# Optimization experiments

Hardware: AMD Instinct MI355X
Metric: run time of the kernel (lower is better)

The kernel has to match this reference:

```python
import jax, jax.numpy as jnp
import numpy as np


def setup_inputs() -> dict:
    key = jax.random.key(0)
    k1, k2, k3 = jax.random.split(key, 3)
    B, T, I, H = 32, 2048, 512, 512
    x = jax.random.normal(k1, (B, T, I), dtype=jnp.float32)
    W_x = jax.random.normal(k2, (3, I, H), dtype=jnp.float32) / np.sqrt(I)
    W_h = jax.random.normal(k3, (3, H, H), dtype=jnp.float32) / np.sqrt(H)
    bias = jnp.zeros((3, H), dtype=jnp.float32)
    return {"x": x, "W_x": W_x, "W_h": W_h, "bias": bias}


def reference(x, W_x, W_h, bias):
    # x: [B, T, I]; W_x: [3, I, H]; W_h: [3, H, H]; bias: [3, H]
    B, T, I = x.shape
    H = W_h.shape[-1]
    # Precompute input-side contributions for all gates/timesteps (batched GEMM):
    # gx: [T, 3, B, H] = x @ W_x[g] + bias[g]
    gx = jnp.einsum('bti,gih->tgbh', x, W_x) + bias[:, None, :]

    W_hz, W_hr, W_hh = W_h[0], W_h[1], W_h[2]

    def step(h_prev, gx_t):
        # gx_t: [3, B, H]
        z = jax.nn.sigmoid(gx_t[0] + h_prev @ W_hz)          # update gate
        r = jax.nn.sigmoid(gx_t[1] + h_prev @ W_hr)          # reset gate
        h_tilde = jnp.tanh(gx_t[2] + (r * h_prev) @ W_hh)    # candidate
        h_t = (1.0 - z) * h_prev + z * h_tilde
        return h_t, h_t

    h0 = jnp.zeros((B, H), dtype=x.dtype)
    h_last, outs = jax.lax.scan(step, h0, gx)  # outs: [T, B, H]
    output = jnp.transpose(outs, (1, 0, 2))    # [B, T, H]
    return output, h_last
```

## Files before the change

kernel.cpp:

```cpp
#include <hip/hip_runtime.h>
#include <stdint.h>
#include <stddef.h>


#define AGENT __HIP_MEMORY_SCOPE_AGENT

typedef _Float16 h2v __attribute__((ext_vector_type(2)));
typedef _Float16 half8 __attribute__((ext_vector_type(8)));
typedef float f32x4 __attribute__((ext_vector_type(4)));

__device__ __forceinline__ uint32_t pk2u(float a, float b) {
  h2v r; r[0] = (_Float16)a; r[1] = (_Float16)b;
  return __builtin_bit_cast(uint32_t, r);
}
__device__ __forceinline__ h2v bc2(uint32_t u) { return __builtin_bit_cast(h2v, u); }
__device__ __forceinline__ float dot2f(h2v a, h2v b, float c) {
#if __has_builtin(__builtin_amdgcn_fdot2)
  return __builtin_amdgcn_fdot2(a, b, c, false);
#else
  return fmaf((float)a[1], (float)b[1], fmaf((float)a[0], (float)b[0], c));
#endif
}
__device__ __forceinline__ float sigmoidf_(float x) { return 1.0f / (1.0f + __expf(-x)); }
__device__ __forceinline__ float tanhf_(float x) { return 1.0f - 2.0f / (1.0f + __expf(2.0f * x)); }
__device__ __forceinline__ uint64_t ald64(const uint64_t* p) {
  return __hip_atomic_load(p, __ATOMIC_RELAXED, AGENT);
}
__device__ __forceinline__ void ast64(uint64_t* p, uint64_t v) {
  __hip_atomic_store(p, v, __ATOMIC_RELAXED, AGENT);
}

__global__ __launch_bounds__(256) void gemm_gx(const float* __restrict__ x,
                                               const float* __restrict__ Wx,
                                               const float* __restrict__ bias,
                                               _Float16* gzr,
                                               _Float16* gh,
                                               int nTN) {
  __shared__ alignas(16) _Float16 Alds[128 * 68];
  __shared__ alignas(16) _Float16 Blds[128 * 68];
  const int tid = threadIdx.x;
  const int bid = blockIdx.x;
  const int tm = bid / nTN, tn = bid % nTN;
  const int m0 = tm << 7, n0 = tn << 7;
  const int lane = tid & 63;
  const int wv = tid >> 6, wm = wv >> 1, wn = wv & 1;
  const int l15 = lane & 15, lhi = lane >> 4;
  f32x4 acc[4][4] = {};

  for (int k0 = 0; k0 < 512; k0 += 64) {
#pragma unroll
    for (int r = 0; r < 8; ++r) {
      int m = r * 16 + (tid >> 4);
      int k = (tid & 15) * 4;
      float4 v = *(const float4*)&x[(size_t)(m0 + m) * 512 + k0 + k];
      union { _Float16 h[4]; uint2 u; } cv;
      cv.h[0] = (_Float16)v.x; cv.h[1] = (_Float16)v.y;
      cv.h[2] = (_Float16)v.z; cv.h[3] = (_Float16)v.w;
      *(uint2*)&Alds[m * 68 + k] = cv.u;
    }
#pragma unroll
    for (int u = 0; u < 8; ++u) {
      int n = tid & 127;
      int k = (tid >> 7) * 32 + u * 4;
      int ng = n0 + n;
      const float* wp = Wx + ((size_t)(ng >> 9) << 18) + (size_t)(k0 + k) * 512 + (ng & 511);
      union { _Float16 h[4]; uint2 u2; } cv;
      cv.h[0] = (_Float16)wp[0];    cv.h[1] = (_Float16)wp[512];
      cv.h[2] = (_Float16)wp[1024]; cv.h[3] = (_Float16)wp[1536];
      *(uint2*)&Blds[n * 68 + k] = cv.u2;
    }
    __syncthreads();
#pragma unroll
    for (int kk = 0; kk < 2; ++kk) {
      int q = kk * 4 + lhi;
      half8 af[4], bf[4];
#pragma unroll
      for (int fm = 0; fm < 4; ++fm) {
        const _Float16* pa = &Alds[(wm * 64 + fm * 16 + l15) * 68 + q * 8];
        union { uint2 u[2]; half8 h; } cv;
        cv.u[0] = *(const uint2*)pa; cv.u[1] = *(const uint2*)(pa + 4);
        af[fm] = cv.h;
      }
#pragma unroll
      for (int fn = 0; fn < 4; ++fn) {
        const _Float16* pb = &Blds[(wn * 64 + fn * 16 + l15) * 68 + q * 8];
        union { uint2 u[2]; half8 h; } cv;
        cv.u[0] = *(const uint2*)pb; cv.u[1] = *(const uint2*)(pb + 4);
        bf[fn] = cv.h;
      }
#pragma unroll
      for (int fm = 0; fm < 4; ++fm)
#pragma unroll
        for (int fn = 0; fn < 4; ++fn)
          acc[fm][fn] = __builtin_amdgcn_mfma_f32_16x16x32_f16(af[fm], bf[fn], acc[fm][fn], 0, 0, 0);
    }
    __syncthreads();
  }
#pragma unroll
  for (int fn = 0; fn < 4; ++fn) {
    int col = n0 + wn * 64 + fn * 16 + l15;
    float bv = bias[col];
#pragma unroll
    for (int fm = 0; fm < 4; ++fm) {
#pragma unroll
      for (int q2 = 0; q2 < 4; ++q2) {
        int row = m0 + wm * 64 + fm * 16 + lhi * 4 + q2;
        _Float16 val = (_Float16)(acc[fm][fn][q2] + bv);
        if (n0 < 1024) gzr[(size_t)row * 1024 + col] = val;
        else           gh[(size_t)row * 512 + (col - 1024)] = val;
      }
    }
  }
}

template <bool GH>
__global__ __launch_bounds__(512) void gru_scan(
    const float* __restrict__ x,
    const float* __restrict__ Wx,
    const float* __restrict__ Wh,
    const float* __restrict__ bias,
    const _Float16* gzr,
    const _Float16* gh,
    float* out,
    uint64_t* __restrict__ Pbuf,
    uint64_t* __restrict__ zbuf) {
  __shared__ alignas(16) float zrp[2][8][64];
  __shared__ alignas(16) _Float16 wzr[2 * 64 * 516];
  __shared__ alignas(16) _Float16 h16[512];
  __shared__ alignas(16) _Float16 rh16[64];
  __shared__ alignas(16) _Float16 x16s[64];

  const int T = threadIdx.x;
  const int bid = blockIdx.x;
  const int xcd = bid & 7, ii = bid >> 3;
  const int batch = xcd * 4 + (ii >> 3);
  const int slice = ii & 7;
  const int wv = T >> 6;
  const int ln = T & 63;
  const int n = T;

  {
    const int cc = T & 63, kb = T >> 6;
#pragma unroll 4
    for (int g = 0; g < 2; ++g) {
      const float* W = Wh + (size_t)g * 262144 + slice * 64 + cc;
      for (int i = 0; i < 64; ++i) {
        int k = kb + 8 * i;
        wzr[(g * 64 + cc) * 516 + k] = (_Float16)W[(size_t)k * 512];
      }
    }
  }
  uint32_t wh2[32], wx2[GH ? 1 : 32];
  {
    const float* Whh = Wh + 524288;
#pragma unroll
    for (int j = 0; j < 32; ++j) {
      int kk = slice * 64 + 2 * j;
      wh2[j] = pk2u(Whh[(size_t)kk * 512 + n], Whh[(size_t)(kk + 1) * 512 + n]);
    }
    if (!GH) {
      const float* Wxh = Wx + 524288;
#pragma unroll
      for (int j = 0; j < 32; ++j) {
        int kk = slice * 64 + 2 * j;
        wx2[j] = pk2u(Wxh[(size_t)kk * 512 + n], Wxh[(size_t)(kk + 1) * 512 + n]);
      }
    }
  }
  const float bh = bias[1024 + n];

  float hreg = 0.0f;
  h16[T] = (_Float16)0.0f;

  const size_t rowbase = (size_t)batch * 2048;
  float gz_p = 0.f, gr_p = 0.f, gz_cur = 0.f, gr_cur = 0.f, x_p = 0.f;
  float gh_p = 0.f, gh_cur = 0.f;
  if (T < 64)       gz_p = (float)gzr[rowbase * 1024 + slice * 64 + T];
  else if (T < 128) gr_p = (float)gzr[rowbase * 1024 + 512 + slice * 64 + (T - 64)];
  if (GH) gh_p = (float)gh[rowbase * 512 + n];
  else if (T < 64) x_p = x[rowbase * 512 + slice * 64 + T];

  uint64_t* Pmine = Pbuf + ((size_t)batch * 8 + slice) * 512 + n;
  const uint64_t* Pread = Pbuf + ((size_t)batch * 8) * 512 + n;
  uint64_t* zmine = zbuf + (size_t)batch * 512 + slice * 64 + ln;
  const uint64_t* zread = zbuf + (size_t)batch * 512 + n;

  for (int t = 0; t < 2048; ++t) {
    if (t > 0) {
      const size_t po = ((t - 1) & 1) ? 131072 : 0;
      const size_t zo = ((t - 1) & 1) ? 16384 : 0;
      const uint32_t want = (uint32_t)t;
      uint64_t v[8];
#pragma unroll
      for (int g = 0; g < 8; ++g) v[g] = ald64(Pread + po + (size_t)g * 512);
      uint64_t zv = ald64(zread + zo);
      for (;;) {
        bool ok = true;
        if ((uint32_t)(zv >> 32) != want) { zv = ald64(zread + zo); ok = false; }
#pragma unroll
        for (int g = 0; g < 8; ++g)
          if ((uint32_t)(v[g] >> 32) != want) { v[g] = ald64(Pread + po + (size_t)g * 512); ok = false; }
        if (ok) break;
        __builtin_amdgcn_s_sleep(1);
      }
      float hsum = 0.f;
#pragma unroll
      for (int g = 0; g < 8; ++g) hsum += __uint_as_float((uint32_t)v[g]);
      float zf = __uint_as_float((uint32_t)zv);
      float htil = tanhf_(GH ? (gh_cur + hsum) : (bh + hsum));
      float hn = fmaf(zf, htil - hreg, hreg);
      if (slice == 0) out[(rowbase + (t - 1)) * 512 + n] = hn;
      hreg = hn;
      h16[T] = (_Float16)hn;
    }
    gz_cur = gz_p; gr_cur = gr_p;
    if (GH) gh_cur = gh_p;
    else if (T < 64) x16s[T] = (_Float16)x_p;
    __syncthreads();
    if (t < 2047) {
      size_t r1 = rowbase + t + 1;
      if (T < 64)       gz_p = (float)gzr[r1 * 1024 + slice * 64 + T];
      else if (T < 128) gr_p = (float)gzr[r1 * 1024 + 512 + slice * 64 + (T - 64)];
      if (GH) gh_p = (float)gh[r1 * 512 + n];
      else if (T < 64) x_p = x[r1 * 512 + slice * 64 + T];
    }

    float za = 0.f, ra = 0.f;
    {
      const _Float16* wzp = &wzr[(0 * 64 + ln) * 516 + 64 * wv];
      const _Float16* wrp = &wzr[(1 * 64 + ln) * 516 + 64 * wv];
      const _Float16* hp = &h16[64 * wv];
#pragma unroll
      for (int j = 0; j < 16; ++j) {
        uint2 wzu = *(const uint2*)(wzp + 4 * j);
        uint2 wru = *(const uint2*)(wrp + 4 * j);
        uint2 hu = *(const uint2*)(hp + 4 * j);
        za = dot2f(bc2(hu.x), bc2(wzu.x), za);
        za = dot2f(bc2(hu.y), bc2(wzu.y), za);
        ra = dot2f(bc2(hu.x), bc2(wru.x), ra);
        ra = dot2f(bc2(hu.y), bc2(wru.y), ra);
      }
    }
    zrp[0][wv][ln] = za;
    zrp[1][wv][ln] = ra;
    __syncthreads();
    const size_t po = (t & 1) ? 131072 : 0;
    const size_t zo = (t & 1) ? 16384 : 0;
    const uint64_t tagw = ((uint64_t)(uint32_t)(t + 1)) << 32;
    if (T < 128) {
      const int g = T >> 6, c = T & 63;
      float sum = 0.f;
#pragma unroll
      for (int s2 = 0; s2 < 8; ++s2) sum += zrp[g][s2][c];
      if (g == 0) {
        float z = sigmoidf_(sum + gz_cur);
        ast64(zmine + zo, tagw | (uint32_t)__float_as_uint(z));
      } else {
        float r = sigmoidf_(sum + gr_cur);
        rh16[c] = (_Float16)(r * (float)h16[slice * 64 + c]);
      }
    }
    __syncthreads();

    float pa = 0.f;
#pragma unroll
    for (int j = 0; j < 16; ++j) {
      uint2 ru = *(const uint2*)&rh16[4 * j];
      pa = dot2f(bc2(ru.x), bc2(wh2[2 * j]), pa);
      pa = dot2f(bc2(ru.y), bc2(wh2[2 * j + 1]), pa);
    }
    if (!GH) {
#pragma unroll
      for (int j = 0; j < 16; ++j) {
        uint2 xu = *(const uint2*)&x16s[4 * j];
        pa = dot2f(bc2(xu.x), bc2(wx2[2 * j]), pa);
        pa = dot2f(bc2(xu.y), bc2(wx2[2 * j + 1]), pa);
      }
    }
    ast64(Pmine + po, tagw | (uint32_t)__float_as_uint(pa));
    if (!GH) __syncthreads();
  }

  {
    const uint32_t want = 2048u;
    uint64_t v[8];
#pragma unroll
    for (int g = 0; g < 8; ++g) v[g] = ald64(Pread + 131072 + (size_t)g * 512);
    uint64_t zv = ald64(zread + 16384);
    for (;;) {
      bool ok = true;
      if ((uint32_t)(zv >> 32) != want) { zv = ald64(zread + 16384); ok = false; }
#pragma unroll
      for (int g = 0; g < 8; ++g)
        if ((uint32_t)(v[g] >> 32) != want) { v[g] = ald64(Pread + 131072 + (size_t)g * 512); ok = false; }
      if (ok) break;
      __builtin_amdgcn_s_sleep(1);
    }
    float hsum = 0.f;
#pragma unroll
    for (int g = 0; g < 8; ++g) hsum += __uint_as_float((uint32_t)v[g]);
    float zf = __uint_as_float((uint32_t)zv);
    float htil = tanhf_(GH ? (gh_cur + hsum) : (bh + hsum));
    float hn = fmaf(zf, htil - hreg, hreg);
    if (slice == 0) {
      out[(rowbase + 2047) * 512 + n] = hn;
      out[(size_t)32 * 2048 * 512 + (size_t)batch * 512 + n] = hn;
    }
  }
}

extern "C" void kernel_launch(void* const* d_in, const int* in_sizes, int n_in,
                              void* d_out, int out_size, void* d_ws, size_t ws_size,
                              hipStream_t stream) {
  (void)in_sizes; (void)n_in; (void)out_size;
  const float* x    = (const float*)d_in[0];
  const float* Wx   = (const float*)d_in[1];
  const float* Wh   = (const float*)d_in[2];
  const float* bias = (const float*)d_in[3];
  float* out = (float*)d_out;
  char* ws = (char*)d_ws;

  uint64_t* Pbuf = (uint64_t*)ws;
  uint64_t* zbuf = (uint64_t*)(ws + 2097152);
  _Float16* gh   = (_Float16*)(ws + 2621440);

  hipMemsetAsync(ws, 0, 2621440, stream);
  const bool gh_mode = ws_size >= (size_t)2621440 + 67108864ull;
  if (gh_mode) {
    gemm_gx<<<512 * 12, 256, 0, stream>>>(x, Wx, bias, (_Float16*)d_out, gh, 12);
    gru_scan<true><<<256, 512, 0, stream>>>(x, Wx, Wh, bias, (const _Float16*)d_out,
                                            gh, out, Pbuf, zbuf);
  } else {
    gemm_gx<<<512 * 8, 256, 0, stream>>>(x, Wx, bias, (_Float16*)d_out, gh, 8);
    gru_scan<false><<<256, 512, 0, stream>>>(x, Wx, Wh, bias, (const _Float16*)d_out,
                                             gh, out, Pbuf, zbuf);
  }
}
```

Before: 7.110 ms.

## Publish candidate partial before z-gate and poll with mostly workgroup-scope loads

Reorders the per-step work so the reset gate and candidate partial are computed and published first, and the update-gate matvec runs after publication. This takes z off the cross-block critical path. Polling now mostly uses workgroup-scope atomic loads, with an agent-scope load every eighth iteration, and publishes store at both workgroup and agent scope. The aim is to cut the cost of cross-CU spin-wait latency. The trade-offs are an extra store per publish and a reliance on scope semantics that may not make remote writes visible promptly, which could lengthen the waits.

```diff
diff --git a/kernel.cpp b/kernel.cpp
--- a/kernel.cpp
+++ b/kernel.cpp
@@ -4,6 +4,7 @@
 
 
 #define AGENT __HIP_MEMORY_SCOPE_AGENT
+#define WGSC  __HIP_MEMORY_SCOPE_WORKGROUP
 
 typedef _Float16 h2v __attribute__((ext_vector_type(2)));
 typedef _Float16 half8 __attribute__((ext_vector_type(8)));
@@ -23,10 +24,13 @@
 }
 __device__ __forceinline__ float sigmoidf_(float x) { return 1.0f / (1.0f + __expf(-x)); }
 __device__ __forceinline__ float tanhf_(float x) { return 1.0f - 2.0f / (1.0f + __expf(2.0f * x)); }
-__device__ __forceinline__ uint64_t ald64(const uint64_t* p) {
-  return __hip_atomic_load(p, __ATOMIC_RELAXED, AGENT);
-}
-__device__ __forceinline__ void ast64(uint64_t* p, uint64_t v) {
+
+__device__ __forceinline__ uint64_t ldT(const uint64_t* p, bool deep) {
+  return deep ? __hip_atomic_load(p, __ATOMIC_RELAXED, AGENT)
+              : __hip_atomic_load(p, __ATOMIC_RELAXED, WGSC);
+}
+__device__ __forceinline__ void pub2(uint64_t* p, uint64_t v) {
+  __hip_atomic_store(p, v, __ATOMIC_RELAXED, WGSC);
   __hip_atomic_store(p, v, __ATOMIC_RELAXED, AGENT);
 }
 
@@ -190,16 +194,16 @@
       const size_t po = ((t - 1) & 1) ? 131072 : 0;
       const size_t zo = ((t - 1) & 1) ? 16384 : 0;
       const uint32_t want = (uint32_t)t;
-      uint64_t v[8];
-#pragma unroll
-      for (int g = 0; g < 8; ++g) v[g] = ald64(Pread + po + (size_t)g * 512);
-      uint64_t zv = ald64(zread + zo);
+      uint64_t v[8] = {};
+      uint64_t zv = 0;
+      int it = 0;
       for (;;) {
         bool ok = true;
-        if ((uint32_t)(zv >> 32) != want) { zv = ald64(zread + zo); ok = false; }
+        bool deep = ((++it) & 7) == 0;
+        if ((uint32_t)(zv >> 32) != want) { zv = ldT(zread + zo, deep); ok = false; }
 #pragma unroll
         for (int g = 0; g < 8; ++g)
-          if ((uint32_t)(v[g] >> 32) != want) { v[g] = ald64(Pread + po + (size_t)g * 512); ok = false; }
+          if ((uint32_t)(v[g] >> 32) != want) { v[g] = ldT(Pread + po + (size_t)g * 512, deep); ok = false; }
         if (ok) break;
         __builtin_amdgcn_s_sleep(1);
       }
@@ -225,40 +229,31 @@
       else if (T < 64) x_p = x[r1 * 512 + slice * 64 + T];
     }
 
-    float za = 0.f, ra = 0.f;
-    {
-      const _Float16* wzp = &wzr[(0 * 64 + ln) * 516 + 64 * wv];
-      const _Float16* wrp = &wzr[(1 * 64 + ln) * 516 + 64 * wv];
-      const _Float16* hp = &h16[64 * wv];
-#pragma unroll
-      for (int j = 0; j < 16; ++j) {
-        uint2 wzu = *(const uint2*)(wzp + 4 * j);
-        uint2 wru = *(const uint2*)(wrp + 4 * j);
-        uint2 hu = *(const uint2*)(hp + 4 * j);
-        za = dot2f(bc2(hu.x), bc2(wzu.x), za);
-        za = dot2f(bc2(hu.y), bc2(wzu.y), za);
-        ra = dot2f(bc2(hu.x), bc2(wru.x), ra);
-        ra = dot2f(bc2(hu.y), bc2(wru.y), ra);
-      }
-    }
-    zrp[0][wv][ln] = za;
-    zrp[1][wv][ln] = ra;
-    __syncthreads();
     const size_t po = (t & 1) ? 131072 : 0;
     const size_t zo = (t & 1) ? 16384 : 0;
     const uint64_t tagw = ((uint64_t)(uint32_t)(t + 1)) << 32;
-    if (T < 128) {
-      const int g = T >> 6, c = T & 63;
+
+    float ra = 0.f;
+    {
+      const _Float16* wrp = &wzr[(64 + ln) * 516 + 64 * wv];
+      const _Float16* hp = &h16[64 * wv];
+#pragma unroll
+      for (int j = 0; j < 16; ++j) {
+        uint2 wru = *(const uint2*)(wrp + 4 * j);
+        uint2 hu = *(const uint2*)(hp + 4 * j);
+        ra = dot2f(bc2(hu.x), bc2(wru.x), ra);
+        ra = dot2f(bc2(hu.y), bc2(wru.y), ra);
+      }
+    }
+    zrp[1][wv][ln] = ra;
+    __syncthreads();
+    if (T >= 64 && T < 128) {
+      const int c = T - 64;
       float sum = 0.f;
 #pragma unroll
-      for (int s2 = 0; s2 < 8; ++s2) sum += zrp[g][s2][c];
-      if (g == 0) {
-        float z = sigmoidf_(sum + gz_cur);
-        ast64(zmine + zo, tagw | (uint32_t)__float_as_uint(z));
-      } else {
-        float r = sigmoidf_(sum + gr_cur);
-        rh16[c] = (_Float16)(r * (float)h16[slice * 64 + c]);
-      }
+      for (int s2 = 0; s2 < 8; ++s2) sum += zrp[1][s2][c];
+      float r = sigmoidf_(sum + gr_cur);
+      rh16[c] = (_Float16)(r * (float)h16[slice * 64 + c]);
     }
     __syncthreads();
 
@@ -277,22 +272,43 @@
         pa = dot2f(bc2(xu.y), bc2(wx2[2 * j + 1]), pa);
       }
     }
-    ast64(Pmine + po, tagw | (uint32_t)__float_as_uint(pa));
-    if (!GH) __syncthreads();
+    pub2(Pmine + po, tagw | (uint32_t)__float_as_uint(pa));
+
+    float za = 0.f;
+    {
+      const _Float16* wzp = &wzr[ln * 516 + 64 * wv];
+      const _Float16* hp = &h16[64 * wv];
+#pragma unroll
+      for (int j = 0; j < 16; ++j) {
+        uint2 wzu = *(const uint2*)(wzp + 4 * j);
+        uint2 hu = *(const uint2*)(hp + 4 * j);
+        za = dot2f(bc2(hu.x), bc2(wzu.x), za);
+        za = dot2f(bc2(hu.y), bc2(wzu.y), za);
+      }
+    }
+    zrp[0][wv][ln] = za;
+    __syncthreads();
+    if (T < 64) {
+      float sum = 0.f;
+#pragma unroll
+      for (int s2 = 0; s2 < 8; ++s2) sum += zrp[0][s2][T];
+      float z = sigmoidf_(sum + gz_cur);
+      pub2(zmine + zo, tagw | (uint32_t)__float_as_uint(z));
+    }
   }
 
   {
     const uint32_t want = 2048u;
     uint64_t v[8];
 #pragma unroll
-    for (int g = 0; g < 8; ++g) v[g] = ald64(Pread + 131072 + (size_t)g * 512);
-    uint64_t zv = ald64(zread + 16384);
+    for (int g = 0; g < 8; ++g) v[g] = ldT(Pread + 131072 + (size_t)g * 512, true);
+    uint64_t zv = ldT(zread + 16384, true);
     for (;;) {
       bool ok = true;
-      if ((uint32_t)(zv >> 32) != want) { zv = ald64(zread + 16384); ok = false; }
+      if ((uint32_t)(zv >> 32) != want) { zv = ldT(zread + 16384, true); ok = false; }
 #pragma unroll
       for (int g = 0; g < 8; ++g)
-        if ((uint32_t)(v[g] >> 32) != want) { v[g] = ald64(Pread + 131072 + (size_t)g * 512); ok = false; }
+        if ((uint32_t)(v[g] >> 32) != want) { v[g] = ldT(Pread + 131072 + (size_t)g * 512, true); ok = false; }
       if (ok) break;
       __builtin_amdgcn_s_sleep(1);
     }
```

Measured after the change: 10.30 ms. +44.8%, slower.

## Interleave two batches per scan block to hide cross-block sync latency

Applied to the files above, without the earlier changes.

Each scan workgroup now processes two independent batch sequences (A and B) in alternating phases, halving the grid from 256 to 128 blocks. While waiting for the other slices' partial sums for one batch, the block does the gate compute for the other, and it issues the flag loads early so they are in flight during that work. This is meant to hide the inter-block spin-wait latency that dominates the recurrent scan. In exchange each block does twice the serial work per step, and the xcd-aware batch mapping is replaced by a plain slice/pair mapping, which may change cache locality.

```diff
diff --git a/kernel.cpp b/kernel.cpp
--- a/kernel.cpp
+++ b/kernel.cpp
@@ -23,11 +23,26 @@
 }
 __device__ __forceinline__ float sigmoidf_(float x) { return 1.0f / (1.0f + __expf(-x)); }
 __device__ __forceinline__ float tanhf_(float x) { return 1.0f - 2.0f / (1.0f + __expf(2.0f * x)); }
-__device__ __forceinline__ uint64_t ald64(const uint64_t* p) {
+
+__device__ __forceinline__ uint64_t ld_agent(const uint64_t* p) {
   return __hip_atomic_load(p, __ATOMIC_RELAXED, AGENT);
 }
-__device__ __forceinline__ void ast64(uint64_t* p, uint64_t v) {
+__device__ __forceinline__ void pub(uint64_t* p, uint64_t v) {
   __hip_atomic_store(p, v, __ATOMIC_RELAXED, AGENT);
+}
+__device__ __forceinline__ void combine_wait(const uint64_t* Pr, const uint64_t* zr,
+                                             uint32_t want, uint64_t v[8], uint64_t& zv) {
+  for (;;) {
+    bool ok = ((uint32_t)(zv >> 32) == want);
+#pragma unroll
+    for (int g = 0; g < 8; ++g) ok &= ((uint32_t)(v[g] >> 32) == want);
+    if (ok) return;
+    __builtin_amdgcn_s_sleep(1);
+    if ((uint32_t)(zv >> 32) != want) zv = ld_agent(zr);
+#pragma unroll
+    for (int g = 0; g < 8; ++g)
+      if ((uint32_t)(v[g] >> 32) != want) v[g] = ld_agent(Pr + (size_t)g * 512);
+  }
 }
 
 __global__ __launch_bounds__(256) void gemm_gx(const float* __restrict__ x,
@@ -126,18 +141,16 @@
     uint64_t* __restrict__ zbuf) {
   __shared__ alignas(16) float zrp[2][8][64];
   __shared__ alignas(16) _Float16 wzr[2 * 64 * 516];
-  __shared__ alignas(16) _Float16 h16[512];
+  __shared__ alignas(16) _Float16 h16A[512], h16B[512];
   __shared__ alignas(16) _Float16 rh16[64];
-  __shared__ alignas(16) _Float16 x16s[64];
+  __shared__ alignas(16) _Float16 x16sA[64], x16sB[64];
 
   const int T = threadIdx.x;
   const int bid = blockIdx.x;
-  const int xcd = bid & 7, ii = bid >> 3;
-  const int batch = xcd * 4 + (ii >> 3);
-  const int slice = ii & 7;
-  const int wv = T >> 6;
-  const int ln = T & 63;
-  const int n = T;
+  const int slice = bid & 7;
+  const int pair = bid >> 3;
+  const int bA = pair;
+  const int wv = T >> 6, ln = T & 63, n = T;
 
   {
     const int cc = T & 63, kb = T >> 6;
@@ -169,67 +182,76 @@
   }
   const float bh = bias[1024 + n];
 
-  float hreg = 0.0f;
-  h16[T] = (_Float16)0.0f;
-
-  const size_t rowbase = (size_t)batch * 2048;
-  float gz_p = 0.f, gr_p = 0.f, gz_cur = 0.f, gr_cur = 0.f, x_p = 0.f;
-  float gh_p = 0.f, gh_cur = 0.f;
-  if (T < 64)       gz_p = (float)gzr[rowbase * 1024 + slice * 64 + T];
-  else if (T < 128) gr_p = (float)gzr[rowbase * 1024 + 512 + slice * 64 + (T - 64)];
-  if (GH) gh_p = (float)gh[rowbase * 512 + n];
-  else if (T < 64) x_p = x[rowbase * 512 + slice * 64 + T];
-
-  uint64_t* Pmine = Pbuf + ((size_t)batch * 8 + slice) * 512 + n;
-  const uint64_t* Pread = Pbuf + ((size_t)batch * 8) * 512 + n;
-  uint64_t* zmine = zbuf + (size_t)batch * 512 + slice * 64 + ln;
-  const uint64_t* zread = zbuf + (size_t)batch * 512 + n;
+  float hregA = 0.f, hregB = 0.f;
+  h16A[T] = (_Float16)0.0f;
+  h16B[T] = (_Float16)0.0f;
+
+  const size_t rbA = (size_t)bA * 2048;
+  const size_t rbB = rbA + (size_t)16 * 2048;
+  float gzA_p = 0.f, grA_p = 0.f, gzA_c = 0.f, grA_c = 0.f, xA_p = 0.f, ghA_p = 0.f, ghA_c = 0.f;
+  float gzB_p = 0.f, grB_p = 0.f, gzB_c = 0.f, grB_c = 0.f, xB_p = 0.f, ghB_p = 0.f, ghB_c = 0.f;
+  if (T < 64) {
+    gzA_p = (float)gzr[rbA * 1024 + slice * 64 + T];
+    gzB_p = (float)gzr[rbB * 1024 + slice * 64 + T];
+  } else if (T < 128) {
+    grA_p = (float)gzr[rbA * 1024 + 512 + slice * 64 + (T - 64)];
+    grB_p = (float)gzr[rbB * 1024 + 512 + slice * 64 + (T - 64)];
+  }
+  if (GH) {
+    ghA_p = (float)gh[rbA * 512 + n];
+    ghB_p = (float)gh[rbB * 512 + n];
+  } else if (T < 64) {
+    xA_p = x[rbA * 512 + slice * 64 + T];
+    xB_p = x[rbB * 512 + slice * 64 + T];
+  }
+
+  uint64_t* PmineA = Pbuf + ((size_t)bA * 8 + slice) * 512 + n;
+  const uint64_t* PreadA = Pbuf + ((size_t)bA * 8) * 512 + n;
+  uint64_t* zmineA = zbuf + (size_t)bA * 512 + slice * 64 + ln;
+  const uint64_t* zreadA = zbuf + (size_t)bA * 512 + n;
+  uint64_t* PmineB = PmineA + 16 * 8 * 512;
+  const uint64_t* PreadB = PreadA + 16 * 8 * 512;
+  uint64_t* zmineB = zmineA + 16 * 512;
+  const uint64_t* zreadB = zreadA + 16 * 512;
+
+  uint64_t vA[8] = {}, vB[8] = {};
+  uint64_t zvA = 0, zvB = 0;
 
   for (int t = 0; t < 2048; ++t) {
+    const size_t poP = ((t - 1) & 1) ? 131072 : 0;
+    const size_t zoP = ((t - 1) & 1) ? 16384 : 0;
+    const size_t po = (t & 1) ? 131072 : 0;
+    const size_t zo = (t & 1) ? 16384 : 0;
+    const uint64_t tagw = ((uint64_t)(uint32_t)(t + 1)) << 32;
+
     if (t > 0) {
-      const size_t po = ((t - 1) & 1) ? 131072 : 0;
-      const size_t zo = ((t - 1) & 1) ? 16384 : 0;
-      const uint32_t want = (uint32_t)t;
-      uint64_t v[8];
-#pragma unroll
-      for (int g = 0; g < 8; ++g) v[g] = ald64(Pread + po + (size_t)g * 512);
-      uint64_t zv = ald64(zread + zo);
-      for (;;) {
-        bool ok = true;
-        if ((uint32_t)(zv >> 32) != want) { zv = ald64(zread + zo); ok = false; }
-#pragma unroll
-        for (int g = 0; g < 8; ++g)
-          if ((uint32_t)(v[g] >> 32) != want) { v[g] = ald64(Pread + po + (size_t)g * 512); ok = false; }
-        if (ok) break;
-        __builtin_amdgcn_s_sleep(1);
-      }
+      combine_wait(PreadA + poP, zreadA + zoP, (uint32_t)t, vA, zvA);
       float hsum = 0.f;
 #pragma unroll
-      for (int g = 0; g < 8; ++g) hsum += __uint_as_float((uint32_t)v[g]);
-      float zf = __uint_as_float((uint32_t)zv);
-      float htil = tanhf_(GH ? (gh_cur + hsum) : (bh + hsum));
-      float hn = fmaf(zf, htil - hreg, hreg);
-      if (slice == 0) out[(rowbase + (t - 1)) * 512 + n] = hn;
-      hreg = hn;
-      h16[T] = (_Float16)hn;
-    }
-    gz_cur = gz_p; gr_cur = gr_p;
-    if (GH) gh_cur = gh_p;
-    else if (T < 64) x16s[T] = (_Float16)x_p;
+      for (int g = 0; g < 8; ++g) hsum += __uint_as_float((uint32_t)vA[g]);
+      float zf = __uint_as_float((uint32_t)zvA);
+      float htil = tanhf_(GH ? (ghA_c + hsum) : (bh + hsum));
+      float hn = fmaf(zf, htil - hregA, hregA);
+      if (slice == 0) out[(rbA + (t - 1)) * 512 + n] = hn;
+      hregA = hn;
+      h16A[T] = (_Float16)hn;
+    }
+    gzA_c = gzA_p; grA_c = grA_p;
+    if (GH) ghA_c = ghA_p;
+    else if (T < 64) x16sA[T] = (_Float16)xA_p;
     __syncthreads();
     if (t < 2047) {
-      size_t r1 = rowbase + t + 1;
-      if (T < 64)       gz_p = (float)gzr[r1 * 1024 + slice * 64 + T];
-      else if (T < 128) gr_p = (float)gzr[r1 * 1024 + 512 + slice * 64 + (T - 64)];
-      if (GH) gh_p = (float)gh[r1 * 512 + n];
-      else if (T < 64) x_p = x[r1 * 512 + slice * 64 + T];
-    }
-
-    float za = 0.f, ra = 0.f;
+      size_t r1 = rbA + t + 1;
+      if (T < 64)       gzA_p = (float)gzr[r1 * 1024 + slice * 64 + T];
+      else if (T < 128) grA_p = (float)gzr[r1 * 1024 + 512 + slice * 64 + (T - 64)];
+      if (GH) ghA_p = (float)gh[r1 * 512 + n];
+      else if (T < 64) xA_p = x[r1 * 512 + slice * 64 + T];
+    }
     {
-      const _Float16* wzp = &wzr[(0 * 64 + ln) * 516 + 64 * wv];
-      const _Float16* wrp = &wzr[(1 * 64 + ln) * 516 + 64 * wv];
-      const _Float16* hp = &h16[64 * wv];
+      float za = 0.f, ra = 0.f;
+      const _Float16* wzp = &wzr[ln * 516 + 64 * wv];
+      const _Float16* wrp = &wzr[(64 + ln) * 516 + 64 * wv];
+      const _Float16* hp = &h16A[64 * wv];
 #pragma unroll
       for (int j = 0; j < 16; ++j) {
         uint2 wzu = *(const uint2*)(wzp + 4 * j);
@@ -240,71 +262,154 @@
         ra = dot2f(bc2(hu.x), bc2(wru.x), ra);
         ra = dot2f(bc2(hu.y), bc2(wru.y), ra);
       }
-    }
-    zrp[0][wv][ln] = za;
-    zrp[1][wv][ln] = ra;
-    __syncthreads();
-    const size_t po = (t & 1) ? 131072 : 0;
-    const size_t zo = (t & 1) ? 16384 : 0;
-    const uint64_t tagw = ((uint64_t)(uint32_t)(t + 1)) << 32;
+      zrp[0][wv][ln] = za;
+      zrp[1][wv][ln] = ra;
+    }
+    __syncthreads();
     if (T < 128) {
       const int g = T >> 6, c = T & 63;
       float sum = 0.f;
 #pragma unroll
       for (int s2 = 0; s2 < 8; ++s2) sum += zrp[g][s2][c];
       if (g == 0) {
-        float z = sigmoidf_(sum + gz_cur);
-        ast64(zmine + zo, tagw | (uint32_t)__float_as_uint(z));
+        pub(zmineA + zo, tagw | (uint32_t)__float_as_uint(sigmoidf_(sum + gzA_c)));
       } else {
-        float r = sigmoidf_(sum + gr_cur);
-        rh16[c] = (_Float16)(r * (float)h16[slice * 64 + c]);
-      }
-    }
-    __syncthreads();
-
-    float pa = 0.f;
-#pragma unroll
-    for (int j = 0; j < 16; ++j) {
-      uint2 ru = *(const uint2*)&rh16[4 * j];
-      pa = dot2f(bc2(ru.x), bc2(wh2[2 * j]), pa);
-      pa = dot2f(bc2(ru.y), bc2(wh2[2 * j + 1]), pa);
-    }
-    if (!GH) {
+        float r = sigmoidf_(sum + grA_c);
+        rh16[c] = (_Float16)(r * (float)h16A[slice * 64 + c]);
+      }
+    }
+    __syncthreads();
+    if (t > 0) {
+#pragma unroll
+      for (int g = 0; g < 8; ++g) vB[g] = ld_agent(PreadB + poP + (size_t)g * 512);
+      zvB = ld_agent(zreadB + zoP);
+      __builtin_amdgcn_sched_barrier(0);
+    }
+    {
+      float pa = 0.f;
 #pragma unroll
       for (int j = 0; j < 16; ++j) {
-        uint2 xu = *(const uint2*)&x16s[4 * j];
-        pa = dot2f(bc2(xu.x), bc2(wx2[2 * j]), pa);
-        pa = dot2f(bc2(xu.y), bc2(wx2[2 * j + 1]), pa);
-      }
-    }
-    ast64(Pmine + po, tagw | (uint32_t)__float_as_uint(pa));
-    if (!GH) __syncthreads();
+        uint2 ru = *(const uint2*)&rh16[4 * j];
+        pa = dot2f(bc2(ru.x), bc2(wh2[2 * j]), pa);
+        pa = dot2f(bc2(ru.y), bc2(wh2[2 * j + 1]), pa);
+      }
+      if (!GH) {
+#pragma unroll
+        for (int j = 0; j < 16; ++j) {
+          uint2 xu = *(const uint2*)&x16sA[4 * j];
+          pa = dot2f(bc2(xu.x), bc2(wx2[2 * j]), pa);
+          pa = dot2f(bc2(xu.y), bc2(wx2[2 * j + 1]), pa);
+        }
+      }
+      pub(PmineA + po, tagw | (uint32_t)__float_as_uint(pa));
+    }
+
+    if (t > 0) {
+      combine_wait(PreadB + poP, zreadB + zoP, (uint32_t)t, vB, zvB);
+      float hsum = 0.f;
+#pragma unroll
+      for (int g = 0; g < 8; ++g) hsum += __uint_as_float((uint32_t)vB[g]);
+      float zf = __uint_as_float((uint32_t)zvB);
+      float htil = tanhf_(GH ? (ghB_c + hsum) : (bh + hsum));
+      float hn = fmaf(zf, htil - hregB, hregB);
+      if (slice == 0) out[(rbB + (t - 1)) * 512 + n] = hn;
+      hregB = hn;
+      h16B[T] = (_Float16)hn;
+    }
+    gzB_c = gzB_p; grB_c = grB_p;
+    if (GH) ghB_c = ghB_p;
+    else if (T < 64) x16sB[T] = (_Float16)xB_p;
+    __syncthreads();
+    if (t < 2047) {
+      size_t r1 = rbB + t + 1;
+      if (T < 64)       gzB_p = (float)gzr[r1 * 1024 + slice * 64 + T];
+      else if (T < 128) grB_p = (float)gzr[r1 * 1024 + 512 + slice * 64 + (T - 64)];
+      if (GH) ghB_p = (float)gh[r1 * 512 + n];
+      else if (T < 64) xB_p = x[r1 * 512 + slice * 64 + T];
+    }
+    {
+      float za = 0.f, ra = 0.f;
+      const _Float16* wzp = &wzr[ln * 516 + 64 * wv];
+      const _Float16* wrp = &wzr[(64 + ln) * 516 + 64 * wv];
+      const _Float16* hp = &h16B[64 * wv];
+#pragma unroll
+      for (int j = 0; j < 16; ++j) {
+        uint2 wzu = *(const uint2*)(wzp + 4 * j);
+        uint2 wru = *(const uint2*)(wrp + 4 * j);
+        uint2 hu = *(const uint2*)(hp + 4 * j);
+        za = dot2f(bc2(hu.x), bc2(wzu.x), za);
+        za = dot2f(bc2(hu.y), bc2(wzu.y), za);
+        ra = dot2f(bc2(hu.x), bc2(wru.x), ra);
+        ra = dot2f(bc2(hu.y), bc2(wru.y), ra);
+      }
+      zrp[0][wv][ln] = za;
+      zrp[1][wv][ln] = ra;
+    }
+    __syncthreads();
+    if (T < 128) {
+      const int g = T >> 6, c = T & 63;
+      float sum = 0.f;
+#pragma unroll
+      for (int s2 = 0; s2 < 8; ++s2) sum += zrp[g][s2][c];
+      if (g == 0) {
+        pub(zmineB + zo, tagw | (uint32_t)__float_as_uint(sigmoidf_(sum + gzB_c)));
+      } else {
+        float r = sigmoidf_(sum + grB_c);
+        rh16[c] = (_Float16)(r * (float)h16B[slice * 64 + c]);
+      }
+    }
+    __syncthreads();
+    {
+      float pa = 0.f;
+#pragma unroll
+      for (int j = 0; j < 16; ++j) {
+        uint2 ru = *(const uint2*)&rh16[4 * j];
+        pa = dot2f(bc2(ru.x), bc2(wh2[2 * j]), pa);
+        pa = dot2f(bc2(ru.y), bc2(wh2[2 * j + 1]), pa);
+      }
+      if (!GH) {
+#pragma unroll
+        for (int j = 0; j < 16; ++j) {
+          uint2 xu = *(const uint2*)&x16sB[4 * j];
+          pa = dot2f(bc2(xu.x), bc2(wx2[2 * j]), pa);
+          pa = dot2f(bc2(xu.y), bc2(wx2[2 * j + 1]), pa);
+        }
+      }
+      pub(PmineB + po, tagw | (uint32_t)__float_as_uint(pa));
+    }
+#pragma unroll
+    for (int g = 0; g < 8; ++g) vA[g] = ld_agent(PreadA + po + (size_t)g * 512);
+    zvA = ld_agent(zreadA + zo);
+    __builtin_amdgcn_sched_barrier(0);
   }
 
   {
-    const uint32_t want = 2048u;
-    uint64_t v[8];
-#pragma unroll
-    for (int g = 0; g < 8; ++g) v[g] = ald64(Pread + 131072 + (size_t)g * 512);
-    uint64_t zv = ald64(zread + 16384);
-    for (;;) {
-      bool ok = true;
-      if ((uint32_t)(zv >> 32) != want) { zv = ald64(zread + 16384); ok = false; }
-#pragma unroll
-      for (int g = 0; g < 8; ++g)
-        if ((uint32_t)(v[g] >> 32) != want) { v[g] = ald64(Pread + 131072 + (size_t)g * 512); ok = false; }
-      if (ok) break;
-      __builtin_amdgcn_s_sleep(1);
-    }
+    combine_wait(PreadA + 131072, zreadA + 16384, 2048u, vA, zvA);
     float hsum = 0.f;
 #pragma unroll
-    for (int g = 0; g < 8; ++g) hsum += __uint_as_float((uint32_t)v[g]);
-    float zf = __uint_as_float((uint32_t)zv);
-    float htil = tanhf_(GH ? (gh_cur + hsum) : (bh + hsum));
-    float hn = fmaf(zf, htil - hreg, hreg);
+    for (int g = 0; g < 8; ++g) hsum += __uint_as_float((uint32_t)vA[g]);
+    float zf = __uint_as_float((uint32_t)zvA);
+    float htil = tanhf_(GH ? (ghA_c + hsum) : (bh + hsum));
+    float hn = fmaf(zf, htil - hregA, hregA);
     if (slice == 0) {
-      out[(rowbase + 2047) * 512 + n] = hn;
-      out[(size_t)32 * 2048 * 512 + (size_t)batch * 512 + n] = hn;
+      out[(rbA + 2047) * 512 + n] = hn;
+      out[(size_t)32 * 2048 * 512 + (size_t)bA * 512 + n] = hn;
+    }
+  }
+  {
+#pragma unroll
+    for (int g = 0; g < 8; ++g) vB[g] = ld_agent(PreadB + 131072 + (size_t)g * 512);
+    zvB = ld_agent(zreadB + 16384);
+    combine_wait(PreadB + 131072, zreadB + 16384, 2048u, vB, zvB);
+    float hsum = 0.f;
+#pragma unroll
+    for (int g = 0; g < 8; ++g) hsum += __uint_as_float((uint32_t)vB[g]);
+    float zf = __uint_as_float((uint32_t)zvB);
+    float htil = tanhf_(GH ? (ghB_c + hsum) : (bh + hsum));
+    float hn = fmaf(zf, htil - hregB, hregB);
+    if (slice == 0) {
+      out[(rbB + 2047) * 512 + n] = hn;
+      out[(size_t)32 * 2048 * 512 + (size_t)(bA + 16) * 512 + n] = hn;
     }
   }
 }
@@ -328,11 +433,11 @@
   const bool gh_mode = ws_size >= (size_t)2621440 + 67108864ull;
   if (gh_mode) {
     gemm_gx<<<512 * 12, 256, 0, stream>>>(x, Wx, bias, (_Float16*)d_out, gh, 12);
-    gru_scan<true><<<256, 512, 0, stream>>>(x, Wx, Wh, bias, (const _Float16*)d_out,
+    gru_scan<true><<<128, 512, 0, stream>>>(x, Wx, Wh, bias, (const _Float16*)d_out,
                                             gh, out, Pbuf, zbuf);
   } else {
     gemm_gx<<<512 * 8, 256, 0, stream>>>(x, Wx, bias, (_Float16*)d_out, gh, 8);
-    gru_scan<false><<<256, 512, 0, stream>>>(x, Wx, Wh, bias, (const _Float16*)d_out,
+    gru_scan<false><<<128, 512, 0, stream>>>(x, Wx, Wh, bias, (const _Float16*)d_out,
                                              gh, out, Pbuf, zbuf);
   }
 }
```

Result: slower. 10.88 ms (+53.0%).

## Replace GRU recurrent scan with MFMA-based kernel batching 16 sequences per block group

Applied to the files above, without the earlier changes.

Adds a new recurrent-scan kernel for the main path. Groups of 16 batch rows share one set of 16 blocks, each block owning 32 hidden columns, and the recurrent matmuls run as 16x16x32 fp16 MFMA tiles with batch as the M dimension. This replaces per-batch dot2 matvecs spread over 256 blocks. Instead of exchanging fp32 partial sums, blocks publish fp16 h and r*h values tagged with the step number and gather them from global memory. The intent is to amortise weight reads across 16 sequences and use matrix cores. The cost is two grid-wide exchanges per step among 16 blocks, and only 32 blocks in total occupy the GPU.

```diff
diff --git a/kernel.cpp b/kernel.cpp
--- a/kernel.cpp
+++ b/kernel.cpp
@@ -23,6 +23,13 @@
 }
 __device__ __forceinline__ float sigmoidf_(float x) { return 1.0f / (1.0f + __expf(-x)); }
 __device__ __forceinline__ float tanhf_(float x) { return 1.0f - 2.0f / (1.0f + __expf(2.0f * x)); }
+
+__device__ __forceinline__ uint32_t ald32(const uint32_t* p) {
+  return __hip_atomic_load(p, __ATOMIC_RELAXED, AGENT);
+}
+__device__ __forceinline__ void ast32(uint32_t* p, uint32_t v) {
+  __hip_atomic_store(p, v, __ATOMIC_RELAXED, AGENT);
+}
 __device__ __forceinline__ uint64_t ald64(const uint64_t* p) {
   return __hip_atomic_load(p, __ATOMIC_RELAXED, AGENT);
 }
@@ -113,19 +120,154 @@
   }
 }
 
+__device__ __forceinline__ void gather16(const uint32_t* base, uint32_t want,
+                                         _Float16* dst) {
+  uint32_t w[16];
+#pragma unroll
+  for (int j = 0; j < 16; ++j) w[j] = ald32(base + j);
+  for (;;) {
+    bool ok = true;
+#pragma unroll
+    for (int j = 0; j < 16; ++j) ok &= ((w[j] >> 16) == want);
+    if (ok) break;
+    __builtin_amdgcn_s_sleep(1);
+#pragma unroll
+    for (int j = 0; j < 16; ++j)
+      if ((w[j] >> 16) != want) w[j] = ald32(base + j);
+  }
+  uint32_t* d32 = (uint32_t*)dst;
+#pragma unroll
+  for (int j = 0; j < 8; ++j)
+    d32[j] = (w[2 * j] & 0xffffu) | (w[2 * j + 1] << 16);
+}
+
+__global__ __launch_bounds__(512) void gru_scan_mfma(
+    const _Float16* gzr,
+    const _Float16* ghg,
+    const float* __restrict__ Wh,
+    float* out,
+    uint32_t* __restrict__ rhbuf,
+    uint32_t* __restrict__ hbuf) {
+  __shared__ alignas(16) _Float16 wzr[64 * 520];
+  __shared__ alignas(16) _Float16 whh[32 * 520];
+  __shared__ alignas(16) _Float16 hA[16 * 520];
+  __shared__ alignas(16) _Float16 rhA[16 * 520];
+  __shared__ alignas(16) float pP[2 * 64 * 20];
+  __shared__ alignas(16) _Float16 gzS[16][32], grS[16][32], ghS[16][32];
+
+  const int tid = threadIdx.x;
+  const int bid = blockIdx.x;
+  const int g = bid >> 4;
+  const int s = bid & 15;
+  const int c0 = s * 32;
+  const int bb = g * 16;
+  const int lane = tid & 63, wv = tid >> 6;
+  const int l15 = lane & 15, lhi = lane >> 4;
+  const int b = tid >> 5, c = tid & 31;
+
+  {
+    const int cc = tid & 31, kb = tid >> 5;
+#pragma unroll 8
+    for (int i = 0; i < 32; ++i) {
+      int k = kb * 32 + i;
+      wzr[cc * 520 + k]        = (_Float16)Wh[(size_t)k * 512 + c0 + cc];
+      wzr[(32 + cc) * 520 + k] = (_Float16)Wh[262144 + (size_t)k * 512 + c0 + cc];
+      whh[cc * 520 + k]        = (_Float16)Wh[524288 + (size_t)k * 512 + c0 + cc];
+    }
+  }
+  for (int i = tid; i < 16 * 520; i += 512) hA[i] = (_Float16)0.0f;
+
+  _Float16 gz_p, gr_p, gh_p;
+  {
+    size_t r0 = (size_t)(bb + b) * 2048;
+    gz_p = gzr[r0 * 1024 + c0 + c];
+    gr_p = gzr[r0 * 1024 + 512 + c0 + c];
+    gh_p = ghg[r0 * 512 + c0 + c];
+  }
+
+  uint32_t* rhb = rhbuf + (size_t)g * 8192;
+  uint32_t* hb  = hbuf + (size_t)g * 8192;
+  const int gw = tid * 16;
+  const int gwb = gw >> 9, gwc = gw & 511;
+
+  for (int t = 0; t < 2048; ++t) {
+    __syncthreads();
+    gzS[b][c] = gz_p; grS[b][c] = gr_p; ghS[b][c] = gh_p;
+    if (t > 0)
+      gather16(hb + gw, (uint32_t)t, &hA[gwb * 520 + gwc]);
+    __syncthreads();
+
+    {
+      const int nt = wv >> 1, kh = wv & 1;
+      f32x4 acc = {};
+#pragma unroll
+      for (int i = 0; i < 8; ++i) {
+        int kc = kh * 8 + i;
+        half8 a = *(const half8*)&hA[l15 * 520 + kc * 32 + lhi * 8];
+        half8 bf = *(const half8*)&wzr[(nt * 16 + l15) * 520 + kc * 32 + lhi * 8];
+        acc = __builtin_amdgcn_mfma_f32_16x16x32_f16(a, bf, acc, 0, 0, 0);
+      }
+      *(f32x4*)&pP[(kh * 64 + nt * 16 + l15) * 20 + lhi * 4] = acc;
+    }
+    if (t < 2047) {
+      size_t r1 = (size_t)(bb + b) * 2048 + t + 1;
+      gz_p = gzr[r1 * 1024 + c0 + c];
+      gr_p = gzr[r1 * 1024 + 512 + c0 + c];
+      gh_p = ghg[r1 * 512 + c0 + c];
+    }
+    __syncthreads();
+
+    float zp = pP[(c)*20 + b] + pP[(64 + c) * 20 + b];
+    float rp = pP[(32 + c) * 20 + b] + pP[(96 + c) * 20 + b];
+    float z = sigmoidf_(zp + (float)gzS[b][c]);
+    float r = sigmoidf_(rp + (float)grS[b][c]);
+    float hold = (float)hA[b * 520 + c0 + c];
+    _Float16 rh16 = (_Float16)(r * hold);
+    rhA[b * 520 + c0 + c] = rh16;
+    ast32(rhb + b * 512 + c0 + c,
+          ((uint32_t)(t + 1) << 16) | (uint32_t)__builtin_bit_cast(unsigned short, rh16));
+
+    gather16(rhb + gw, (uint32_t)(t + 1), &rhA[gwb * 520 + gwc]);
+    __syncthreads();
+
+    {
+      const int nt = wv >> 2, kq = wv & 3;
+      f32x4 acc = {};
+#pragma unroll
+      for (int i = 0; i < 4; ++i) {
+        int kc = kq * 4 + i;
+        half8 a = *(const half8*)&rhA[l15 * 520 + kc * 32 + lhi * 8];
+        half8 bf = *(const half8*)&whh[(nt * 16 + l15) * 520 + kc * 32 + lhi * 8];
+        acc = __builtin_amdgcn_mfma_f32_16x16x32_f16(a, bf, acc, 0, 0, 0);
+      }
+      *(f32x4*)&pP[(kq * 32 + nt * 16 + l15) * 20 + lhi * 4] = acc;
+    }
+    __syncthreads();
+
+    {
+      float hp = pP[(c)*20 + b] + pP[(32 + c) * 20 + b] +
+                 pP[(64 + c) * 20 + b] + pP[(96 + c) * 20 + b];
+      float htil = tanhf_(hp + (float)ghS[b][c]);
+      float hn = fmaf(z, htil - hold, hold);
+      out[((size_t)(bb + b) * 2048 + t) * 512 + c0 + c] = hn;
+      _Float16 h16v = (_Float16)hn;
+      hA[b * 520 + c0 + c] = h16v;
+      ast32(hb + b * 512 + c0 + c,
+            ((uint32_t)(t + 1) << 16) | (uint32_t)__builtin_bit_cast(unsigned short, h16v));
+      if (t == 2047)
+        out[(size_t)32 * 2048 * 512 + (size_t)(bb + b) * 512 + c0 + c] = hn;
+    }
+  }
+}
+
 template <bool GH>
-__global__ __launch_bounds__(512) void gru_scan(
-    const float* __restrict__ x,
-    const float* __restrict__ Wx,
-    const float* __restrict__ Wh,
-    const float* __restrict__ bias,
-    const _Float16* gzr,
-    const _Float16* gh,
-    float* out,
-    uint64_t* __restrict__ Pbuf,
-    uint64_t* __restrict__ zbuf) {
+__global__ __launch_bounds__(512) void gru_scan_fb(
+    const float* __restrict__ x, const float* __restrict__ Wx,
+    const float* __restrict__ Wh, const float* __restrict__ bias,
+    const _Float16* gzr, const _Float16* gh, float* out,
+    uint64_t* __restrict__ Pbuf, uint64_t* __restrict__ zbuf) {
   __shared__ alignas(16) float zrp[2][8][64];
-  __shared__ alignas(16) _Float16 wzr[2 * 64 * 516];
+  __shared__ alignas(16) _Float16 wzrL[2 * 64 * 516];
   __shared__ alignas(16) _Float16 h16[512];
   __shared__ alignas(16) _Float16 rh16[64];
   __shared__ alignas(16) _Float16 x16s[64];
@@ -135,10 +277,7 @@
   const int xcd = bid & 7, ii = bid >> 3;
   const int batch = xcd * 4 + (ii >> 3);
   const int slice = ii & 7;
-  const int wv = T >> 6;
-  const int ln = T & 63;
-  const int n = T;
-
+  const int wv = T >> 6, ln = T & 63, n = T;
   {
     const int cc = T & 63, kb = T >> 6;
 #pragma unroll 4
@@ -146,39 +285,29 @@
       const float* W = Wh + (size_t)g * 262144 + slice * 64 + cc;
       for (int i = 0; i < 64; ++i) {
         int k = kb + 8 * i;
-        wzr[(g * 64 + cc) * 516 + k] = (_Float16)W[(size_t)k * 512];
-      }
-    }
-  }
-  uint32_t wh2[32], wx2[GH ? 1 : 32];
+        wzrL[(g * 64 + cc) * 516 + k] = (_Float16)W[(size_t)k * 512];
+      }
+    }
+  }
+  uint32_t wh2[32], wx2[32];
   {
     const float* Whh = Wh + 524288;
+    const float* Wxh = Wx + 524288;
 #pragma unroll
     for (int j = 0; j < 32; ++j) {
       int kk = slice * 64 + 2 * j;
       wh2[j] = pk2u(Whh[(size_t)kk * 512 + n], Whh[(size_t)(kk + 1) * 512 + n]);
-    }
-    if (!GH) {
-      const float* Wxh = Wx + 524288;
-#pragma unroll
-      for (int j = 0; j < 32; ++j) {
-        int kk = slice * 64 + 2 * j;
-        wx2[j] = pk2u(Wxh[(size_t)kk * 512 + n], Wxh[(size_t)(kk + 1) * 512 + n]);
-      }
+      wx2[j] = pk2u(Wxh[(size_t)kk * 512 + n], Wxh[(size_t)(kk + 1) * 512 + n]);
     }
   }
   const float bh = bias[1024 + n];
-
   float hreg = 0.0f;
   h16[T] = (_Float16)0.0f;
-
   const size_t rowbase = (size_t)batch * 2048;
   float gz_p = 0.f, gr_p = 0.f, gz_cur = 0.f, gr_cur = 0.f, x_p = 0.f;
-  float gh_p = 0.f, gh_cur = 0.f;
   if (T < 64)       gz_p = (float)gzr[rowbase * 1024 + slice * 64 + T];
   else if (T < 128) gr_p = (float)gzr[rowbase * 1024 + 512 + slice * 64 + (T - 64)];
-  if (GH) gh_p = (float)gh[rowbase * 512 + n];
-  else if (T < 64) x_p = x[rowbase * 512 + slice * 64 + T];
+  if (T < 64) x_p = x[rowbase * 512 + slice * 64 + T];
 
   uint64_t* Pmine = Pbuf + ((size_t)batch * 8 + slice) * 512 + n;
   const uint64_t* Pread = Pbuf + ((size_t)batch * 8) * 512 + n;
@@ -207,28 +336,25 @@
 #pragma unroll
       for (int g = 0; g < 8; ++g) hsum += __uint_as_float((uint32_t)v[g]);
       float zf = __uint_as_float((uint32_t)zv);
-      float htil = tanhf_(GH ? (gh_cur + hsum) : (bh + hsum));
+      float htil = tanhf_(bh + hsum);
       float hn = fmaf(zf, htil - hreg, hreg);
       if (slice == 0) out[(rowbase + (t - 1)) * 512 + n] = hn;
       hreg = hn;
       h16[T] = (_Float16)hn;
     }
     gz_cur = gz_p; gr_cur = gr_p;
-    if (GH) gh_cur = gh_p;
-    else if (T < 64) x16s[T] = (_Float16)x_p;
+    if (T < 64) x16s[T] = (_Float16)x_p;
     __syncthreads();
     if (t < 2047) {
       size_t r1 = rowbase + t + 1;
       if (T < 64)       gz_p = (float)gzr[r1 * 1024 + slice * 64 + T];
       else if (T < 128) gr_p = (float)gzr[r1 * 1024 + 512 + slice * 64 + (T - 64)];
-      if (GH) gh_p = (float)gh[r1 * 512 + n];
-      else if (T < 64) x_p = x[r1 * 512 + slice * 64 + T];
-    }
-
+      if (T < 64) x_p = x[r1 * 512 + slice * 64 + T];
+    }
     float za = 0.f, ra = 0.f;
     {
-      const _Float16* wzp = &wzr[(0 * 64 + ln) * 516 + 64 * wv];
-      const _Float16* wrp = &wzr[(1 * 64 + ln) * 516 + 64 * wv];
+      const _Float16* wzp = &wzrL[ln * 516 + 64 * wv];
+      const _Float16* wrp = &wzrL[(64 + ln) * 516 + 64 * wv];
       const _Float16* hp = &h16[64 * wv];
 #pragma unroll
       for (int j = 0; j < 16; ++j) {
@@ -248,20 +374,19 @@
     const size_t zo = (t & 1) ? 16384 : 0;
     const uint64_t tagw = ((uint64_t)(uint32_t)(t + 1)) << 32;
     if (T < 128) {
-      const int g = T >> 6, c = T & 63;
+      const int g = T >> 6, cc = T & 63;
       float sum = 0.f;
 #pragma unroll
-      for (int s2 = 0; s2 < 8; ++s2) sum += zrp[g][s2][c];
+      for (int s2 = 0; s2 < 8; ++s2) sum += zrp[g][s2][cc];
       if (g == 0) {
         float z = sigmoidf_(sum + gz_cur);
         ast64(zmine + zo, tagw | (uint32_t)__float_as_uint(z));
       } else {
         float r = sigmoidf_(sum + gr_cur);
-        rh16[c] = (_Float16)(r * (float)h16[slice * 64 + c]);
-      }
-    }
-    __syncthreads();
-
+        rh16[cc] = (_Float16)(r * (float)h16[slice * 64 + cc]);
+      }
+    }
+    __syncthreads();
     float pa = 0.f;
 #pragma unroll
     for (int j = 0; j < 16; ++j) {
@@ -269,18 +394,15 @@
       pa = dot2f(bc2(ru.x), bc2(wh2[2 * j]), pa);
       pa = dot2f(bc2(ru.y), bc2(wh2[2 * j + 1]), pa);
     }
-    if (!GH) {
-#pragma unroll
-      for (int j = 0; j < 16; ++j) {
-        uint2 xu = *(const uint2*)&x16s[4 * j];
-        pa = dot2f(bc2(xu.x), bc2(wx2[2 * j]), pa);
-        pa = dot2f(bc2(xu.y), bc2(wx2[2 * j + 1]), pa);
-      }
+#pragma unroll
+    for (int j = 0; j < 16; ++j) {
+      uint2 xu = *(const uint2*)&x16s[4 * j];
+      pa = dot2f(bc2(xu.x), bc2(wx2[2 * j]), pa);
+      pa = dot2f(bc2(xu.y), bc2(wx2[2 * j + 1]), pa);
     }
     ast64(Pmine + po, tagw | (uint32_t)__float_as_uint(pa));
-    if (!GH) __syncthreads();
-  }
-
+    __syncthreads();
+  }
   {
     const uint32_t want = 2048u;
     uint64_t v[8];
@@ -300,7 +422,7 @@
 #pragma unroll
     for (int g = 0; g < 8; ++g) hsum += __uint_as_float((uint32_t)v[g]);
     float zf = __uint_as_float((uint32_t)zv);
-    float htil = tanhf_(GH ? (gh_cur + hsum) : (bh + hsum));
+    float htil = tanhf_(bh + hsum);
     float hn = fmaf(zf, htil - hreg, hreg);
     if (slice == 0) {
       out[(rowbase + 2047) * 512 + n] = hn;
@@ -320,19 +442,22 @@
   float* out = (float*)d_out;
   char* ws = (char*)d_ws;
 
-  uint64_t* Pbuf = (uint64_t*)ws;
-  uint64_t* zbuf = (uint64_t*)(ws + 2097152);
-  _Float16* gh   = (_Float16*)(ws + 2621440);
+  uint32_t* rhbuf = (uint32_t*)ws;
+  uint32_t* hbuf  = (uint32_t*)(ws + 65536);
+  uint64_t* Pbuf  = (uint64_t*)ws;
+  uint64_t* zbuf  = (uint64_t*)(ws + 2097152);
+  _Float16* gh    = (_Float16*)(ws + 2621440);
 
   hipMemsetAsync(ws, 0, 2621440, stream);
   const bool gh_mode = ws_size >= (size_t)2621440 + 67108864ull;
   if (gh_mode) {
     gemm_gx<<<512 * 12, 256, 0, stream>>>(x, Wx, bias, (_Float16*)d_out, gh, 12);
-    gru_scan<true><<<256, 512, 0, stream>>>(x, Wx, Wh, bias, (const _Float16*)d_out,
-                                            gh, out, Pbuf, zbuf);
+    gru_scan_mfma<<<32, 512, 0, stream>>>((const _Float16*)d_out, gh, Wh, out,
+                                          rhbuf, hbuf);
   } else {
     gemm_gx<<<512 * 8, 256, 0, stream>>>(x, Wx, bias, (_Float16*)d_out, gh, 8);
-    gru_scan<false><<<256, 512, 0, stream>>>(x, Wx, Wh, bias, (const _Float16*)d_out,
-                                             gh, out, Pbuf, zbuf);
-  }
-}
+    gru_scan_fb<false><<<256, 512, 0, stream>>>(x, Wx, Wh, bias,
+                                                (const _Float16*)d_out, gh, out,
+                                                Pbuf, zbuf);
+  }
+}
```

Result: slower. 28.31 ms (+298.2%).
